# Optimization experiments

Measured on AMD Instinct MI355X. Metric: run time of the kernel, lower is better.

The kernel has to match this reference:

```python
import jax, jax.numpy as jnp
import numpy as np
import math

N_HEADS = 32
N_KV_HEADS = 4
HEAD_DIM = 128
N_REP = N_HEADS // N_KV_HEADS
ROPE_THETA = 10000.0
YARN_SCALE = 80.0
YARN_ALPHA = 1.0
YARN_BETA = 32.0
MAX_SEQ = int(2048 * YARN_SCALE)  # max_seq_len * yarn_scale, as in __init__


def _rope_yarn_cos_sin(S, dim):
    """Numpy (static) version of precompute_rope_yarn, sliced to S positions."""
    inv_freq = 1.0 / ROPE_THETA ** (np.arange(0, dim, 2, dtype=np.float32) / dim)
    wavelengths = 2.0 * math.pi / inv_freq
    r = MAX_SEQ / wavelengths
    gamma = np.clip((r - YARN_ALPHA) / (YARN_BETA - YARN_ALPHA), 0.0, 1.0)
    inv_freq = inv_freq * ((1.0 - gamma) / YARN_SCALE + gamma)
    t = np.arange(S, dtype=np.float32)
    freqs = np.outer(t, inv_freq)                      # [S, dim/2]
    emb = np.concatenate([freqs, freqs], axis=-1)      # [S, dim]
    emb = emb / math.sqrt(0.1 * math.log(YARN_SCALE) + 1.0)
    # broadcast shape [1, S, 1, dim] to apply per-position across heads
    return (jnp.asarray(np.cos(emb))[None, :, None, :],
            jnp.asarray(np.sin(emb))[None, :, None, :])


def _rotate_half(x):
    x1, x2 = jnp.split(x, 2, axis=-1)
    return jnp.concatenate([-x2, x1], axis=-1)


def setup_inputs() -> dict:
    key = jax.random.key(0)
    ks = jax.random.split(key, 5)
    B, S, D = 1, 2048, 4096
    sd = 1.0 / math.sqrt(D)
    return {
        "x": jax.random.normal(ks[0], (B, S, D), dtype=jnp.float32),
        "wq": jax.random.normal(ks[1], (D, N_HEADS * HEAD_DIM), dtype=jnp.float32) * sd,
        "wk": jax.random.normal(ks[2], (D, N_KV_HEADS * HEAD_DIM), dtype=jnp.float32) * sd,
        "wv": jax.random.normal(ks[3], (D, N_KV_HEADS * HEAD_DIM), dtype=jnp.float32) * sd,
        "wo": jax.random.normal(ks[4], (N_HEADS * HEAD_DIM, D), dtype=jnp.float32) * sd,
    }


def reference(x, wq, wk, wv, wo):
    B, S, D = x.shape
    scale = HEAD_DIM ** -0.5
    q = (x @ wq).reshape(B, S, N_HEADS, HEAD_DIM)
    k = (x @ wk).reshape(B, S, N_KV_HEADS, HEAD_DIM)
    v = (x @ wv).reshape(B, S, N_KV_HEADS, HEAD_DIM)
    cos, sin = _rope_yarn_cos_sin(S, HEAD_DIM)         # [1,S,1,Dh]
    q = q * cos + _rotate_half(q) * sin
    k = k * cos + _rotate_half(k) * sin
    # GQA: repeat kv heads to match query heads (repeat_interleave on head dim)
    k = jnp.repeat(k, N_REP, axis=2)
    v = jnp.repeat(v, N_REP, axis=2)
    # [B,H,S,Dh]
    q = q.transpose(0, 2, 1, 3)
    k = k.transpose(0, 2, 1, 3)
    v = v.transpose(0, 2, 1, 3)
    scores = jnp.einsum("bhsd,bhtd->bhst", q, k) * scale
    causal = jnp.tril(jnp.ones((S, S), dtype=bool))
    scores = jnp.where(causal[None, None], scores, jnp.finfo(scores.dtype).min)
    probs = jax.nn.softmax(scores, axis=-1)
    out = jnp.einsum("bhst,bhtd->bhsd", probs, v)
    out = out.transpose(0, 2, 1, 3).reshape(B, S, N_HEADS * HEAD_DIM)
    return out @ wo
```

## Files before the change

kernel.cpp:

```cpp
#include <hip/hip_runtime.h>
#include <math.h>

#define S_LEN 2048
#define D_MODEL 4096
#define NH 32
#define NKV 4
#define HD 128
#define KV_W (NKV * HD)
#define QK_W (D_MODEL + KV_W)
#define QKV_W (QK_W + KV_W)

typedef float f32x4 __attribute__((ext_vector_type(4)));
typedef __bf16 bf16x8 __attribute__((ext_vector_type(8)));

__device__ __forceinline__ void async16(const __bf16* g, __bf16* l) {
    __builtin_amdgcn_global_load_lds(
        (const __attribute__((address_space(1))) unsigned int*)g,
        (__attribute__((address_space(3))) unsigned int*)l, 16, 0, 0);
}

__global__ void cast_f32_bf16(const float* __restrict__ in, __bf16* __restrict__ out, int n) {
    int i = (blockIdx.x * blockDim.x + threadIdx.x) * 4;
    if (i >= n) return;
    float4 v = *reinterpret_cast<const float4*>(in + i);
    out[i + 0] = (__bf16)v.x;
    out[i + 1] = (__bf16)v.y;
    out[i + 2] = (__bf16)v.z;
    out[i + 3] = (__bf16)v.w;
}

__global__ void transpose_cast(const float* __restrict__ in, __bf16* __restrict__ out, int R, int C) {
    __shared__ float tile[64][65];
    const int tid = threadIdx.x;
    const int bx = blockIdx.x * 64, by = blockIdx.y * 64;
#pragma unroll
    for (int i = 0; i < 4; i++) {
        int idx = tid + i * 256;
        int r = idx >> 4, c4 = (idx & 15) * 4;
        float4 v = *(const float4*)(in + (size_t)(by + r) * C + bx + c4);
        tile[r][c4 + 0] = v.x; tile[r][c4 + 1] = v.y;
        tile[r][c4 + 2] = v.z; tile[r][c4 + 3] = v.w;
    }
    __syncthreads();
#pragma unroll
    for (int i = 0; i < 2; i++) {
        int idx = tid + i * 256;
        int oc = idx >> 3, r8 = (idx & 7) * 8;
        bf16x8 v;
#pragma unroll
        for (int e = 0; e < 8; e++) v[e] = (__bf16)tile[r8 + e][oc];
        *(bf16x8*)(out + (size_t)(bx + oc) * R + by + r8) = v;
    }
}

template <int MODE>
__global__ __launch_bounds__(256, 2) void gemm_bf16(const __bf16* __restrict__ A,
                                                    const __bf16* __restrict__ Bt,
                                                    void* __restrict__ Cp, void* __restrict__ Cp2,
                                                    int M, int N, int K) {
    __shared__ __bf16 a_lds[2][128 * 32];
    __shared__ __bf16 b_lds[2][128 * 32];

    const int tid = threadIdx.x;
    const int wave = tid >> 6, lane = tid & 63;
    const int quad = lane >> 4, l16 = lane & 15;
    const int wm = wave & 1, wn = wave >> 1;
    const int m0 = blockIdx.y * 128, n0 = blockIdx.x * 128;

    f32x4 acc[4][4];
#pragma unroll
    for (int i = 0; i < 4; i++)
#pragma unroll
        for (int j = 0; j < 4; j++) acc[i][j] = (f32x4)0.0f;

    const int crow = tid >> 2, ccol = (tid & 3) * 8;
    const __bf16* Ap0 = A + (size_t)(m0 + crow) * K + ccol;
    const __bf16* Ap1 = A + (size_t)(m0 + 64 + crow) * K + ccol;
    const __bf16* Bp0 = Bt + (size_t)(n0 + crow) * K + ccol;
    const __bf16* Bp1 = Bt + (size_t)(n0 + 64 + crow) * K + ccol;

    async16(Ap0, a_lds[0] + tid * 8);
    async16(Ap1, a_lds[0] + (tid + 256) * 8);
    async16(Bp0, b_lds[0] + tid * 8);
    async16(Bp1, b_lds[0] + (tid + 256) * 8);

    for (int k0 = 0; k0 < K; k0 += 32) {
        const int cur = (k0 >> 5) & 1;
        __syncthreads();
        if (k0 + 32 < K) {
            async16(Ap0 + k0 + 32, a_lds[cur ^ 1] + tid * 8);
            async16(Ap1 + k0 + 32, a_lds[cur ^ 1] + (tid + 256) * 8);
            async16(Bp0 + k0 + 32, b_lds[cur ^ 1] + tid * 8);
            async16(Bp1 + k0 + 32, b_lds[cur ^ 1] + (tid + 256) * 8);
        }

        bf16x8 afr[4], bfr[4];
#pragma unroll
        for (int i = 0; i < 4; i++)
            afr[i] = *(const bf16x8*)(a_lds[cur] + (wm * 64 + i * 16 + l16) * 32 + quad * 8);
#pragma unroll
        for (int j = 0; j < 4; j++)
            bfr[j] = *(const bf16x8*)(b_lds[cur] + (wn * 64 + j * 16 + l16) * 32 + quad * 8);
#pragma unroll
        for (int i = 0; i < 4; i++)
#pragma unroll
            for (int j = 0; j < 4; j++)
                acc[i][j] = __builtin_amdgcn_mfma_f32_16x16x32_bf16(afr[i], bfr[j], acc[i][j], 0, 0, 0);
    }

    const bool vregion = (MODE == 1) && (n0 >= QK_W);
#pragma unroll
    for (int i = 0; i < 4; i++)
#pragma unroll
        for (int j = 0; j < 4; j++)
#pragma unroll
            for (int r = 0; r < 4; r++) {
                int gm = m0 + wm * 64 + i * 16 + quad * 4 + r;
                int gn = n0 + wn * 64 + j * 16 + l16;
                float v = acc[i][j][r];
                if constexpr (MODE == 0) {
                    ((float*)Cp)[(size_t)gm * N + gn] = v;
                } else {
                    if (vregion)
                        ((__bf16*)Cp2)[(size_t)(gn - QK_W) * M + gm] = (__bf16)v;
                    else
                        ((__bf16*)Cp)[(size_t)gm * QK_W + gn] = (__bf16)v;
                }
            }
}

__global__ void rope_cast(const __bf16* __restrict__ src, int sPitch, int sOff,
                          __bf16* __restrict__ dst, int dPitch, int H, int total) {
    int idx = blockIdx.x * blockDim.x + threadIdx.x;
    if (idx >= total) return;
    int d = idx & 63;
    int t = idx >> 6;
    int h = t % H;
    int s = t / H;

    float inv = __powf(10000.0f, -(float)d * (1.0f / 64.0f));
    float wl = 6.2831853071795864f / inv;
    float r = 163840.0f / wl;
    float gamma = fminf(fmaxf((r - 1.0f) * (1.0f / 31.0f), 0.0f), 1.0f);
    float adj = inv * ((1.0f - gamma) * (1.0f / 80.0f) + gamma);
    float ang = ((float)s * adj) / 1.1992508365439246f;
    float c = cosf(ang), sn = sinf(ang);

    const __bf16* b = src + (size_t)s * sPitch + sOff + h * HD;
    __bf16* o = dst + (size_t)s * dPitch + h * HD;
    float x1 = (float)b[d], x2 = (float)b[d + 64];
    o[d] = (__bf16)(x1 * c - x2 * sn);
    o[d + 64] = (__bf16)(x2 * c + x1 * sn);
}

__global__ __launch_bounds__(256, 2) void flash_attn(const __bf16* __restrict__ Q,
                                                     const __bf16* __restrict__ Kb,
                                                     const __bf16* __restrict__ Vt,
                                                     __bf16* __restrict__ O) {
    __shared__ __bf16 k_lds[2][64 * 128];
    __shared__ __bf16 vt_lds[128 * 64];
    __shared__ __bf16 p_lds[128 * 72];

    const int tid = threadIdx.x;
    const int wave = tid >> 6, lane = tid & 63;
    const int quad = lane >> 4, l16 = lane & 15;
    const int h = blockIdx.x;
    const int ty = blockIdx.y;
    const int t = (ty < 8) ? ty : 23 - ty;
    const int qb0 = t * 128;
    const int wrow = wave * 32;
    const int kvh = h >> 3;
    const float sl2e = 0.12752039149672056f;

    bf16x8 qfr[2][4];
#pragma unroll
    for (int mi = 0; mi < 2; mi++)
#pragma unroll
        for (int kk = 0; kk < 4; kk++)
            qfr[mi][kk] = *(const bf16x8*)(Q + (size_t)(qb0 + wrow + mi * 16 + l16) * D_MODEL
                                           + h * HD + kk * 32 + quad * 8);

    f32x4 acc[2][8];
#pragma unroll
    for (int mi = 0; mi < 2; mi++)
#pragma unroll
        for (int dt = 0; dt < 8; dt++) acc[mi][dt] = (f32x4)0.0f;
    float rs[2][4] = {{0.f, 0.f, 0.f, 0.f}, {0.f, 0.f, 0.f, 0.f}};

    const int nk = 2 * t + 2;

#pragma unroll
    for (int it = 0; it < 4; it++) {
        int c = tid + it * 256;
        int krow = c >> 4, kcb = c & 15;
        async16(Kb + (size_t)krow * KV_W + kvh * HD + ((kcb ^ (krow & 15)) << 3),
                k_lds[0] + c * 8);
    }
    __syncthreads();

    for (int kt = 0; kt < nk; kt++) {
        const int k0 = kt * 64;
        const int cur = kt & 1;

#pragma unroll
        for (int it = 0; it < 4; it++) {
            int c = tid + it * 256;
            int vrow = c >> 3, vcb = c & 7;
            async16(Vt + (size_t)(kvh * HD + vrow) * S_LEN + k0 + ((vcb ^ (vrow & 7)) << 3),
                    vt_lds + c * 8);
        }

        f32x4 sc[2][4];
#pragma unroll
        for (int mi = 0; mi < 2; mi++)
#pragma unroll
            for (int j = 0; j < 4; j++) sc[mi][j] = (f32x4)0.0f;
#pragma unroll
        for (int j = 0; j < 4; j++)
#pragma unroll
            for (int kk = 0; kk < 4; kk++) {
                bf16x8 kf = *(const bf16x8*)(k_lds[cur] + (((j * 16 + l16) << 4) + ((kk * 4 + quad) ^ l16)) * 8);
                sc[0][j] = __builtin_amdgcn_mfma_f32_16x16x32_bf16(qfr[0][kk], kf, sc[0][j], 0, 0, 0);
                sc[1][j] = __builtin_amdgcn_mfma_f32_16x16x32_bf16(qfr[1][kk], kf, sc[1][j], 0, 0, 0);
            }

        const bool hasmask = (kt >= 2 * t);
#pragma unroll
        for (int mi = 0; mi < 2; mi++) {
            int rowb = qb0 + wrow + mi * 16 + quad * 4;
#pragma unroll
            for (int j = 0; j < 4; j++) {
                int kg = k0 + j * 16 + l16;
#pragma unroll
                for (int r = 0; r < 4; r++) {
                    float p = __builtin_amdgcn_exp2f(sc[mi][j][r] * sl2e);
                    if (hasmask && kg > rowb + r) p = 0.0f;
                    rs[mi][r] += p;
                    p_lds[(wrow + mi * 16 + quad * 4 + r) * 72 + j * 16 + l16] = (__bf16)p;
                }
            }
        }

        __syncthreads();

        if (kt + 1 < nk) {
#pragma unroll
            for (int it = 0; it < 4; it++) {
                int c = tid + it * 256;
                int krow = c >> 4, kcb = c & 15;
                async16(Kb + (size_t)(k0 + 64 + krow) * KV_W + kvh * HD + ((kcb ^ (krow & 15)) << 3),
                        k_lds[cur ^ 1] + c * 8);
            }
        }

        bf16x8 pf[2][2];
#pragma unroll
        for (int mi = 0; mi < 2; mi++)
#pragma unroll
            for (int kk = 0; kk < 2; kk++)
                pf[mi][kk] = *(const bf16x8*)(p_lds + (wrow + mi * 16 + l16) * 72 + kk * 32 + quad * 8);
#pragma unroll
        for (int dt = 0; dt < 8; dt++)
#pragma unroll
            for (int kk = 0; kk < 2; kk++) {
                bf16x8 vf = *(const bf16x8*)(vt_lds + (((dt * 16 + l16) << 3) + ((kk * 4 + quad) ^ (l16 & 7))) * 8);
                acc[0][dt] = __builtin_amdgcn_mfma_f32_16x16x32_bf16(pf[0][kk], vf, acc[0][dt], 0, 0, 0);
                acc[1][dt] = __builtin_amdgcn_mfma_f32_16x16x32_bf16(pf[1][kk], vf, acc[1][dt], 0, 0, 0);
            }

        __syncthreads();
    }

    float inv_l[2][4];
#pragma unroll
    for (int mi = 0; mi < 2; mi++)
#pragma unroll
        for (int r = 0; r < 4; r++) {
            float s = rs[mi][r];
#pragma unroll
            for (int m = 1; m <= 8; m <<= 1) s += __shfl_xor(s, m, 64);
            inv_l[mi][r] = 1.0f / s;
        }

#pragma unroll
    for (int mi = 0; mi < 2; mi++)
#pragma unroll
        for (int dt = 0; dt < 8; dt++)
#pragma unroll
            for (int r = 0; r < 4; r++) {
                int row = qb0 + wrow + mi * 16 + quad * 4 + r;
                int col = h * HD + dt * 16 + l16;
                O[(size_t)row * D_MODEL + col] = (__bf16)(acc[mi][dt][r] * inv_l[mi][r]);
            }
}

extern "C" void kernel_launch(void* const* d_in, const int* in_sizes, int n_in,
                              void* d_out, int out_size, void* d_ws, size_t ws_size,
                              hipStream_t stream) {
    const float* x = (const float*)d_in[0];
    const float* wq = (const float*)d_in[1];
    const float* wk = (const float*)d_in[2];
    const float* wv = (const float*)d_in[3];
    const float* wo = (const float*)d_in[4];
    float* out = (float*)d_out;

    char* ws = (char*)d_ws;
    size_t off = 0;
    auto alloc = [&](size_t bytes) {
        void* p = ws + off;
        off += (bytes + 255) & ~(size_t)255;
        return p;
    };
    __bf16* xb    = (__bf16*)alloc((size_t)S_LEN * D_MODEL * 2);
    __bf16* wqkvT = (__bf16*)alloc((size_t)QKV_W * D_MODEL * 2);
    __bf16* woT   = (__bf16*)alloc((size_t)D_MODEL * D_MODEL * 2);
    __bf16* qkb   = (__bf16*)alloc((size_t)S_LEN * QK_W * 2);
    __bf16* vtb   = (__bf16*)alloc((size_t)KV_W * S_LEN * 2);
    __bf16* qb    = (__bf16*)alloc((size_t)S_LEN * D_MODEL * 2);
    __bf16* kb    = (__bf16*)alloc((size_t)S_LEN * KV_W * 2);
    __bf16* ob    = (__bf16*)alloc((size_t)S_LEN * D_MODEL * 2);

    cast_f32_bf16<<<(S_LEN * D_MODEL) / (256 * 4), 256, 0, stream>>>(x, xb, S_LEN * D_MODEL);
    transpose_cast<<<dim3(D_MODEL / 64, D_MODEL / 64), 256, 0, stream>>>(wq, wqkvT, D_MODEL, D_MODEL);
    transpose_cast<<<dim3(KV_W / 64, D_MODEL / 64), 256, 0, stream>>>(wk, wqkvT + (size_t)D_MODEL * D_MODEL, D_MODEL, KV_W);
    transpose_cast<<<dim3(KV_W / 64, D_MODEL / 64), 256, 0, stream>>>(wv, wqkvT + (size_t)QK_W * D_MODEL, D_MODEL, KV_W);
    transpose_cast<<<dim3(D_MODEL / 64, D_MODEL / 64), 256, 0, stream>>>(wo, woT, D_MODEL, D_MODEL);

    gemm_bf16<1><<<dim3(QKV_W / 128, S_LEN / 128), 256, 0, stream>>>(xb, wqkvT, qkb, vtb, S_LEN, QKV_W, D_MODEL);

    rope_cast<<<(S_LEN * NH * 64) / 256, 256, 0, stream>>>(qkb, QK_W, 0, qb, D_MODEL, NH, S_LEN * NH * 64);
    rope_cast<<<(S_LEN * NKV * 64) / 256, 256, 0, stream>>>(qkb, QK_W, D_MODEL, kb, KV_W, NKV, S_LEN * NKV * 64);

    flash_attn<<<dim3(NH, 16), 256, 0, stream>>>(qb, kb, vtb, ob);

    gemm_bf16<0><<<dim3(D_MODEL / 128, S_LEN / 128), 256, 0, stream>>>(ob, woT, out, nullptr, S_LEN, D_MODEL, D_MODEL);
}
```

Baseline: 494.2 us.

## Replace 128x128 GEMM with 256x256 phased, swizzled, pipelined GEMM kernel

Replaces the projection GEMM with a 512-thread kernel computing 256x256 tiles. It uses a 64-deep K step, an XOR-swizzled LDS layout, and a four-phase schedule that interleaves async staging of the next tiles with MFMA work, plus a workgroup id remap. The goal is more operand reuse per LDS load and fewer bank conflicts and stalls. The risk is that larger tiles leave fewer workgroups than CUs and use 128KB LDS, which limits occupancy. It also adds s_setprio around the MFMA blocks in flash attention.

Result: slower. 589.7 us (+19.3%).

```diff
diff --git a/kernel.cpp b/kernel.cpp
--- a/kernel.cpp
+++ b/kernel.cpp
@@ -54,69 +54,113 @@
 }
 
 template <int MODE>
-__global__ __launch_bounds__(256, 2) void gemm_bf16(const __bf16* __restrict__ A,
-                                                    const __bf16* __restrict__ Bt,
-                                                    void* __restrict__ Cp, void* __restrict__ Cp2,
-                                                    int M, int N, int K) {
-    __shared__ __bf16 a_lds[2][128 * 32];
-    __shared__ __bf16 b_lds[2][128 * 32];
+__global__ __launch_bounds__(512, 2) void gemm256(const __bf16* __restrict__ A,
+                                                  const __bf16* __restrict__ Bt,
+                                                  void* __restrict__ Cp, void* __restrict__ Cp2,
+                                                  int M, int N, int K) {
+    __shared__ __bf16 aL[2][256 * 64];
+    __shared__ __bf16 bL[2][256 * 64];
 
     const int tid = threadIdx.x;
     const int wave = tid >> 6, lane = tid & 63;
     const int quad = lane >> 4, l16 = lane & 15;
-    const int wm = wave & 1, wn = wave >> 1;
-    const int m0 = blockIdx.y * 128, n0 = blockIdx.x * 128;
-
-    f32x4 acc[4][4];
-#pragma unroll
-    for (int i = 0; i < 4; i++)
+    const int wm = wave >> 2, wn = wave & 3;
+
+    const int gx = gridDim.x;
+    const int nwg = gx * gridDim.y;
+    int id = blockIdx.y * gx + blockIdx.x;
+    id = (id & 7) * (nwg >> 3) + (id >> 3);
+    const int n0 = (id % gx) * 256, m0 = (id / gx) * 256;
+
+    const int NT = K >> 6;
+
+    const int srow = tid >> 3;
+    const int schunk = (tid & 7) ^ (srow & 7);
+    const __bf16* pA = A + (size_t)(m0 + srow) * K + schunk * 8;
+    const __bf16* pB = Bt + (size_t)(n0 + srow) * K + schunk * 8;
+
+    auto stageA = [&](int buf, int h, int kt) {
+#pragma unroll
+        for (int b = 0; b < 2; ++b)
+            async16(pA + (size_t)(h * 128 + b * 64) * K + kt * 64,
+                    &aL[buf][(h * 128 + b * 64) * 64 + tid * 8]);
+    };
+    auto stageB = [&](int buf, int h, int kt) {
+#pragma unroll
+        for (int b = 0; b < 2; ++b)
+            async16(pB + (size_t)(h * 128 + b * 64) * K + kt * 64,
+                    &bL[buf][(h * 128 + b * 64) * 64 + tid * 8]);
+    };
+
+    f32x4 acc[8][4];
+#pragma unroll
+    for (int i = 0; i < 8; i++)
 #pragma unroll
         for (int j = 0; j < 4; j++) acc[i][j] = (f32x4)0.0f;
 
-    const int crow = tid >> 2, ccol = (tid & 3) * 8;
-    const __bf16* Ap0 = A + (size_t)(m0 + crow) * K + ccol;
-    const __bf16* Ap1 = A + (size_t)(m0 + 64 + crow) * K + ccol;
-    const __bf16* Bp0 = Bt + (size_t)(n0 + crow) * K + ccol;
-    const __bf16* Bp1 = Bt + (size_t)(n0 + 64 + crow) * K + ccol;
-
-    async16(Ap0, a_lds[0] + tid * 8);
-    async16(Ap1, a_lds[0] + (tid + 256) * 8);
-    async16(Bp0, b_lds[0] + tid * 8);
-    async16(Bp1, b_lds[0] + (tid + 256) * 8);
-
-    for (int k0 = 0; k0 < K; k0 += 32) {
-        const int cur = (k0 >> 5) & 1;
-        __syncthreads();
-        if (k0 + 32 < K) {
-            async16(Ap0 + k0 + 32, a_lds[cur ^ 1] + tid * 8);
-            async16(Ap1 + k0 + 32, a_lds[cur ^ 1] + (tid + 256) * 8);
-            async16(Bp0 + k0 + 32, b_lds[cur ^ 1] + tid * 8);
-            async16(Bp1 + k0 + 32, b_lds[cur ^ 1] + (tid + 256) * 8);
-        }
-
-        bf16x8 afr[4], bfr[4];
-#pragma unroll
-        for (int i = 0; i < 4; i++)
-            afr[i] = *(const bf16x8*)(a_lds[cur] + (wm * 64 + i * 16 + l16) * 32 + quad * 8);
+    const int arow0 = wm * 64 + l16;
+    const int brow0 = wn * 32 + l16;
+    const int ach0 = ((0 + quad) ^ (l16 & 7)) * 8;
+    const int ach1 = ((4 + quad) ^ (l16 & 7)) * 8;
+
+    stageA(0, 0, 0); stageB(0, 0, 0);
+    stageA(0, 1, 0); stageB(0, 1, 0);
+    stageA(1, 0, 1); stageB(1, 0, 1);
+    asm volatile("s_waitcnt vmcnt(4)" ::: "memory");
+    __builtin_amdgcn_sched_barrier(0);
+    __builtin_amdgcn_s_barrier();
+
+#define GPHASE(QM, QN, STAGE_STMT, END_STMT)                                             \
+    {                                                                                    \
+        bf16x8 af[4][2], bf[2][2];                                                       \
+        _Pragma("unroll") for (int mi = 0; mi < 4; ++mi) {                               \
+            const __bf16* ab = &aL[cur][((QM)*128 + arow0 + mi * 16) * 64];              \
+            af[mi][0] = *(const bf16x8*)(ab + ach0);                                     \
+            af[mi][1] = *(const bf16x8*)(ab + ach1);                                     \
+        }                                                                                \
+        _Pragma("unroll") for (int ni = 0; ni < 2; ++ni) {                               \
+            const __bf16* bb = &bL[cur][((QN)*128 + brow0 + ni * 16) * 64];              \
+            bf[ni][0] = *(const bf16x8*)(bb + ach0);                                     \
+            bf[ni][1] = *(const bf16x8*)(bb + ach1);                                     \
+        }                                                                                \
+        STAGE_STMT                                                                       \
+        __builtin_amdgcn_s_barrier();                                                    \
+        asm volatile("s_waitcnt lgkmcnt(0)" ::: "memory");                               \
+        __builtin_amdgcn_sched_barrier(0);                                               \
+        __builtin_amdgcn_s_setprio(1);                                                   \
+        _Pragma("unroll") for (int mi = 0; mi < 4; ++mi)                                 \
+            _Pragma("unroll") for (int ni = 0; ni < 2; ++ni) {                           \
+                acc[(QM)*4 + mi][(QN)*2 + ni] = __builtin_amdgcn_mfma_f32_16x16x32_bf16( \
+                    af[mi][0], bf[ni][0], acc[(QM)*4 + mi][(QN)*2 + ni], 0, 0, 0);       \
+                acc[(QM)*4 + mi][(QN)*2 + ni] = __builtin_amdgcn_mfma_f32_16x16x32_bf16( \
+                    af[mi][1], bf[ni][1], acc[(QM)*4 + mi][(QN)*2 + ni], 0, 0, 0);       \
+            }                                                                            \
+        __builtin_amdgcn_s_setprio(0);                                                   \
+        END_STMT                                                                         \
+        __builtin_amdgcn_s_barrier();                                                    \
+    }
+
+    for (int g = 0; g < NT; ++g) {
+        const int cur = g & 1, nxt = cur ^ 1;
+        GPHASE(0, 0, if (g + 1 < NT) stageA(nxt, 1, g + 1);, )
+        GPHASE(0, 1, if (g + 1 < NT) stageB(nxt, 1, g + 1);, )
+        GPHASE(1, 0, if (g + 2 < NT) stageA(cur, 0, g + 2);, )
+        GPHASE(1, 1, if (g + 2 < NT) stageB(cur, 0, g + 2);,
+               if (g + 2 < NT) { asm volatile("s_waitcnt vmcnt(4)" ::: "memory"); }
+               else if (g + 1 < NT) { asm volatile("s_waitcnt vmcnt(0)" ::: "memory"); }
+               __builtin_amdgcn_sched_barrier(0);)
+    }
+#undef GPHASE
+
+    const bool vregion = (MODE == 1) && (n0 >= QK_W);
+#pragma unroll
+    for (int i = 0; i < 8; i++)
 #pragma unroll
         for (int j = 0; j < 4; j++)
-            bfr[j] = *(const bf16x8*)(b_lds[cur] + (wn * 64 + j * 16 + l16) * 32 + quad * 8);
-#pragma unroll
-        for (int i = 0; i < 4; i++)
-#pragma unroll
-            for (int j = 0; j < 4; j++)
-                acc[i][j] = __builtin_amdgcn_mfma_f32_16x16x32_bf16(afr[i], bfr[j], acc[i][j], 0, 0, 0);
-    }
-
-    const bool vregion = (MODE == 1) && (n0 >= QK_W);
-#pragma unroll
-    for (int i = 0; i < 4; i++)
-#pragma unroll
-        for (int j = 0; j < 4; j++)
 #pragma unroll
             for (int r = 0; r < 4; r++) {
-                int gm = m0 + wm * 64 + i * 16 + quad * 4 + r;
-                int gn = n0 + wn * 64 + j * 16 + l16;
+                int gm = m0 + (i >> 2) * 128 + wm * 64 + (i & 3) * 16 + quad * 4 + r;
+                int gn = n0 + (j >> 1) * 128 + wn * 32 + (j & 1) * 16 + l16;
                 float v = acc[i][j][r];
                 if constexpr (MODE == 0) {
                     ((float*)Cp)[(size_t)gm * N + gn] = v;
@@ -215,6 +259,7 @@
         for (int mi = 0; mi < 2; mi++)
 #pragma unroll
             for (int j = 0; j < 4; j++) sc[mi][j] = (f32x4)0.0f;
+        __builtin_amdgcn_s_setprio(1);
 #pragma unroll
         for (int j = 0; j < 4; j++)
 #pragma unroll
@@ -223,6 +268,7 @@
                 sc[0][j] = __builtin_amdgcn_mfma_f32_16x16x32_bf16(qfr[0][kk], kf, sc[0][j], 0, 0, 0);
                 sc[1][j] = __builtin_amdgcn_mfma_f32_16x16x32_bf16(qfr[1][kk], kf, sc[1][j], 0, 0, 0);
             }
+        __builtin_amdgcn_s_setprio(0);
 
         const bool hasmask = (kt >= 2 * t);
 #pragma unroll
@@ -259,6 +305,7 @@
 #pragma unroll
             for (int kk = 0; kk < 2; kk++)
                 pf[mi][kk] = *(const bf16x8*)(p_lds + (wrow + mi * 16 + l16) * 72 + kk * 32 + quad * 8);
+        __builtin_amdgcn_s_setprio(1);
 #pragma unroll
         for (int dt = 0; dt < 8; dt++)
 #pragma unroll
@@ -267,6 +314,7 @@
                 acc[0][dt] = __builtin_amdgcn_mfma_f32_16x16x32_bf16(pf[0][kk], vf, acc[0][dt], 0, 0, 0);
                 acc[1][dt] = __builtin_amdgcn_mfma_f32_16x16x32_bf16(pf[1][kk], vf, acc[1][dt], 0, 0, 0);
             }
+        __builtin_amdgcn_s_setprio(0);
 
         __syncthreads();
     }
@@ -326,12 +374,12 @@
     transpose_cast<<<dim3(KV_W / 64, D_MODEL / 64), 256, 0, stream>>>(wv, wqkvT + (size_t)QK_W * D_MODEL, D_MODEL, KV_W);
     transpose_cast<<<dim3(D_MODEL / 64, D_MODEL / 64), 256, 0, stream>>>(wo, woT, D_MODEL, D_MODEL);
 
-    gemm_bf16<1><<<dim3(QKV_W / 128, S_LEN / 128), 256, 0, stream>>>(xb, wqkvT, qkb, vtb, S_LEN, QKV_W, D_MODEL);
+    gemm256<1><<<dim3(QKV_W / 256, S_LEN / 256), 512, 0, stream>>>(xb, wqkvT, qkb, vtb, S_LEN, QKV_W, D_MODEL);
 
     rope_cast<<<(S_LEN * NH * 64) / 256, 256, 0, stream>>>(qkb, QK_W, 0, qb, D_MODEL, NH, S_LEN * NH * 64);
     rope_cast<<<(S_LEN * NKV * 64) / 256, 256, 0, stream>>>(qkb, QK_W, D_MODEL, kb, KV_W, NKV, S_LEN * NKV * 64);
 
     flash_attn<<<dim3(NH, 16), 256, 0, stream>>>(qb, kb, vtb, ob);
 
-    gemm_bf16<0><<<dim3(D_MODEL / 128, S_LEN / 128), 256, 0, stream>>>(ob, woT, out, nullptr, S_LEN, D_MODEL, D_MODEL);
-}
+    gemm256<0><<<dim3(D_MODEL / 256, S_LEN / 256), 512, 0, stream>>>(ob, woT, out, nullptr, S_LEN, D_MODEL, D_MODEL);
+}
```

## Double-buffer V tiles, prefetch K/V ahead and drop a per-iteration barrier

Applied to the files above, without the earlier changes.

The flash-attention loop now double-buffers the V tile alongside K. It issues both next-tile loads at the top of each iteration and waits on them only once at the end, behind a single barrier instead of two. The P staging buffer drops its padding for an XOR swizzle, and each wave reads back only the rows it wrote, so the intermediate block barrier is removed. The MFMA sections are wrapped in s_setprio raises. The added V buffer increases LDS use, which may limit how many blocks fit per CU.

Result: slower. 515.0 us (+4.2%).

```diff
diff --git a/kernel.cpp b/kernel.cpp
--- a/kernel.cpp
+++ b/kernel.cpp
@@ -158,8 +158,8 @@
                                                      const __bf16* __restrict__ Vt,
                                                      __bf16* __restrict__ O) {
     __shared__ __bf16 k_lds[2][64 * 128];
-    __shared__ __bf16 vt_lds[128 * 64];
-    __shared__ __bf16 p_lds[128 * 72];
+    __shared__ __bf16 vt_lds[2][128 * 64];
+    __shared__ __bf16 p_lds[128 * 64];
 
     const int tid = threadIdx.x;
     const int wave = tid >> 6, lane = tid & 63;
@@ -189,25 +189,46 @@
 
     const int nk = 2 * t + 2;
 
+    const int kc = tid, krow = kc >> 2, kcb0 = kc & 3;
+    (void)kc; (void)krow; (void)kcb0;
+
 #pragma unroll
     for (int it = 0; it < 4; it++) {
         int c = tid + it * 256;
-        int krow = c >> 4, kcb = c & 15;
-        async16(Kb + (size_t)krow * KV_W + kvh * HD + ((kcb ^ (krow & 15)) << 3),
+        int kr = c >> 4, kb = c & 15;
+        async16(Kb + (size_t)kr * KV_W + kvh * HD + ((kb ^ (kr & 15)) << 3),
                 k_lds[0] + c * 8);
     }
-    __syncthreads();
+#pragma unroll
+    for (int it = 0; it < 4; it++) {
+        int c = tid + it * 256;
+        int vr = c >> 3, vb = c & 7;
+        async16(Vt + (size_t)(kvh * HD + vr) * S_LEN + 0 + ((vb ^ (vr & 7)) << 3),
+                vt_lds[0] + c * 8);
+    }
+    asm volatile("s_waitcnt vmcnt(0)" ::: "memory");
+    __builtin_amdgcn_sched_barrier(0);
+    __builtin_amdgcn_s_barrier();
 
     for (int kt = 0; kt < nk; kt++) {
         const int k0 = kt * 64;
         const int cur = kt & 1;
 
-#pragma unroll
-        for (int it = 0; it < 4; it++) {
-            int c = tid + it * 256;
-            int vrow = c >> 3, vcb = c & 7;
-            async16(Vt + (size_t)(kvh * HD + vrow) * S_LEN + k0 + ((vcb ^ (vrow & 7)) << 3),
-                    vt_lds + c * 8);
+        if (kt + 1 < nk) {
+#pragma unroll
+            for (int it = 0; it < 4; it++) {
+                int c = tid + it * 256;
+                int kr = c >> 4, kb = c & 15;
+                async16(Kb + (size_t)(k0 + 64 + kr) * KV_W + kvh * HD + ((kb ^ (kr & 15)) << 3),
+                        k_lds[cur ^ 1] + c * 8);
+            }
+#pragma unroll
+            for (int it = 0; it < 4; it++) {
+                int c = tid + it * 256;
+                int vr = c >> 3, vb = c & 7;
+                async16(Vt + (size_t)(kvh * HD + vr) * S_LEN + (k0 + 64) + ((vb ^ (vr & 7)) << 3),
+                        vt_lds[cur ^ 1] + c * 8);
+            }
         }
 
         f32x4 sc[2][4];
@@ -215,6 +236,7 @@
         for (int mi = 0; mi < 2; mi++)
 #pragma unroll
             for (int j = 0; j < 4; j++) sc[mi][j] = (f32x4)0.0f;
+        __builtin_amdgcn_s_setprio(1);
 #pragma unroll
         for (int j = 0; j < 4; j++)
 #pragma unroll
@@ -223,6 +245,7 @@
                 sc[0][j] = __builtin_amdgcn_mfma_f32_16x16x32_bf16(qfr[0][kk], kf, sc[0][j], 0, 0, 0);
                 sc[1][j] = __builtin_amdgcn_mfma_f32_16x16x32_bf16(qfr[1][kk], kf, sc[1][j], 0, 0, 0);
             }
+        __builtin_amdgcn_s_setprio(0);
 
         const bool hasmask = (kt >= 2 * t);
 #pragma unroll
@@ -236,39 +259,35 @@
                     float p = __builtin_amdgcn_exp2f(sc[mi][j][r] * sl2e);
                     if (hasmask && kg > rowb + r) p = 0.0f;
                     rs[mi][r] += p;
-                    p_lds[(wrow + mi * 16 + quad * 4 + r) * 72 + j * 16 + l16] = (__bf16)p;
+                    int pr = wrow + mi * 16 + quad * 4 + r;
+                    int ch = (2 * j + (l16 >> 3)) ^ (pr & 7);
+                    p_lds[pr * 64 + ch * 8 + (l16 & 7)] = (__bf16)p;
                 }
             }
         }
 
-        __syncthreads();
-
-        if (kt + 1 < nk) {
-#pragma unroll
-            for (int it = 0; it < 4; it++) {
-                int c = tid + it * 256;
-                int krow = c >> 4, kcb = c & 15;
-                async16(Kb + (size_t)(k0 + 64 + krow) * KV_W + kvh * HD + ((kcb ^ (krow & 15)) << 3),
-                        k_lds[cur ^ 1] + c * 8);
-            }
-        }
-
         bf16x8 pf[2][2];
 #pragma unroll
         for (int mi = 0; mi < 2; mi++)
 #pragma unroll
-            for (int kk = 0; kk < 2; kk++)
-                pf[mi][kk] = *(const bf16x8*)(p_lds + (wrow + mi * 16 + l16) * 72 + kk * 32 + quad * 8);
+            for (int kk = 0; kk < 2; kk++) {
+                int row = wrow + mi * 16 + l16;
+                pf[mi][kk] = *(const bf16x8*)(p_lds + row * 64 + (((kk * 4 + quad) ^ (row & 7)) << 3));
+            }
+        __builtin_amdgcn_s_setprio(1);
 #pragma unroll
         for (int dt = 0; dt < 8; dt++)
 #pragma unroll
             for (int kk = 0; kk < 2; kk++) {
-                bf16x8 vf = *(const bf16x8*)(vt_lds + (((dt * 16 + l16) << 3) + ((kk * 4 + quad) ^ (l16 & 7))) * 8);
+                bf16x8 vf = *(const bf16x8*)(vt_lds[cur] + (((dt * 16 + l16) << 3) + ((kk * 4 + quad) ^ (l16 & 7))) * 8);
                 acc[0][dt] = __builtin_amdgcn_mfma_f32_16x16x32_bf16(pf[0][kk], vf, acc[0][dt], 0, 0, 0);
                 acc[1][dt] = __builtin_amdgcn_mfma_f32_16x16x32_bf16(pf[1][kk], vf, acc[1][dt], 0, 0, 0);
             }
-
-        __syncthreads();
+        __builtin_amdgcn_s_setprio(0);
+
+        if (kt + 1 < nk) { asm volatile("s_waitcnt vmcnt(0)" ::: "memory"); }
+        __builtin_amdgcn_sched_barrier(0);
+        __builtin_amdgcn_s_barrier();
     }
 
     float inv_l[2][4];
```
